# Kernel optimization log

Measured on AMD Instinct MI355X. Metric: run time of the kernel, lower is better.

## Reference

```python
import jax, jax.numpy as jnp
import numpy as np

B, S, D_IN, D_MODEL, H = 4, 2048, 1024, 1024, 16
HD = D_MODEL // H  # 64


def setup_inputs() -> dict:
    key = jax.random.key(0)
    k1, k2, k3, k4, k5 = jax.random.split(key, 5)
    x = jax.random.normal(k1, (B, S, D_IN), dtype=jnp.float32)
    mask = jnp.zeros((1, 1, S, S), dtype=jnp.float32)  # additive mask
    # qkv_layer: Linear(D_IN, 3*D_MODEL)
    W_qkv = jax.random.normal(k2, (D_IN, 3 * D_MODEL), dtype=jnp.float32) / np.sqrt(D_IN)
    b_qkv = jax.random.normal(k3, (3 * D_MODEL,), dtype=jnp.float32) * 0.01
    # linear_layer: Linear(D_MODEL, D_MODEL)
    W_o = jax.random.normal(k4, (D_MODEL, D_MODEL), dtype=jnp.float32) / np.sqrt(D_MODEL)
    b_o = jax.random.normal(k5, (D_MODEL,), dtype=jnp.float32) * 0.01
    return {"x": x, "mask": mask, "W_qkv": W_qkv, "b_qkv": b_qkv, "W_o": W_o, "b_o": b_o}


def reference(x, mask, W_qkv, b_qkv, W_o, b_o):
    b, s, _ = x.shape
    qkv = x @ W_qkv + b_qkv                                  # [B,S,3*D]
    qkv = qkv.reshape(b, s, H, 3 * HD).transpose(0, 2, 1, 3)  # [B,H,S,3*HD]
    q, k, v = jnp.split(qkv, 3, axis=-1)                     # each [B,H,S,HD]
    scale = 1.0 / jnp.sqrt(jnp.asarray(HD, dtype=q.dtype))
    scores = jnp.einsum('bhqd,bhkd->bhqk', q, k) * scale + mask  # [B,H,S,S]
    attn = jax.nn.softmax(scores, axis=-1)
    values = jnp.einsum('bhqk,bhkd->bhqd', attn, v)           # [B,H,S,HD]
    values = values.transpose(0, 2, 1, 3).reshape(b, s, H * HD)  # [B,S,D]
    out = values @ W_o + b_o
    return (out, values)
```

## Files before the change

kernel.cpp:

```cpp
#include <hip/hip_runtime.h>
#include <hip/hip_bf16.h>


typedef __attribute__((ext_vector_type(8))) short short8;
typedef __attribute__((ext_vector_type(4))) float f32x4;

#define SCL2E 0.1803368801111204f
#define L2E   1.44269504088896340736f

#define GLD16(g, l)                                                            \
  __builtin_amdgcn_global_load_lds(                                            \
      (const __attribute__((address_space(1))) unsigned int*)(g),              \
      (__attribute__((address_space(3))) unsigned int*)(l), 16, 0, 0)

__device__ __forceinline__ unsigned short f2b(float f) {
  union { float f; unsigned int u; } v; v.f = f;
  unsigned int u = v.u;
  return (unsigned short)((u + 0x7fffu + ((u >> 16) & 1u)) >> 16);
}
__device__ __forceinline__ unsigned int fbits(float f) {
  union { float f; unsigned int u; } v; v.f = f; return v.u;
}
__device__ __forceinline__ unsigned int cvt_pk_bf16(float lo, float hi) {
  unsigned int r;
  asm("v_cvt_pk_bf16_f32 %0, %1, %2" : "=v"(r) : "v"(lo), "v"(hi));
  return r;
}
__device__ __forceinline__ float max3f(float a, float b, float c) {
  return fmaxf(fmaxf(a, b), c);
}

__global__ void prep(const float* __restrict__ in, ushort* __restrict__ out,
                     const float* __restrict__ mask,
                     unsigned char* __restrict__ mflagsB) {
  const int bid = blockIdx.x;
  if (bid < 8192) {
    int i = (bid * 256 + threadIdx.x) * 4;
    float4 f = *(const float4*)(in + i);
    ushort4 o;
    o.x = f2b(f.x); o.y = f2b(f.y); o.z = f2b(f.z); o.w = f2b(f.w);
    *(ushort4*)(out + i) = o;
    return;
  }
  __shared__ unsigned int s;
  const int t = bid - 8192;
  const int qt = t >> 4, kt = t & 15;
  const float* base = mask + (size_t)(qt * 128) * 2048 + kt * 128;
  const int row = threadIdx.x >> 1, col0 = (threadIdx.x & 1) * 64;
  unsigned int acc = 0;
#pragma unroll
  for (int i = 0; i < 16; ++i) {
    float4 f = *(const float4*)(base + (size_t)row * 2048 + col0 + i * 4);
    acc |= fbits(f.x) | fbits(f.y) | fbits(f.z) | fbits(f.w);
  }
  acc &= 0x7fffffffu;
  if (threadIdx.x == 0) s = 0u;
  __syncthreads();
  if (acc) atomicOr(&s, 1u);
  __syncthreads();
  if (threadIdx.x == 0) mflagsB[t] = s ? 1 : 0;
}

__global__ void transpose_cvt2(const float* __restrict__ W1, ushort* __restrict__ Wt1,
                               const float* __restrict__ W2, ushort* __restrict__ Wt2) {
  __shared__ float tile[64][65];
  const int bx = blockIdx.x;
  const float* W; ushort* Wt; int N, n0;
  if (bx < 48) { W = W1; Wt = Wt1; N = 3072; n0 = bx * 64; }
  else         { W = W2; Wt = Wt2; N = 1024; n0 = (bx - 48) * 64; }
  const int K = 1024, k0 = blockIdx.y * 64;
  int tx = threadIdx.x & 63, ty = threadIdx.x >> 6;
#pragma unroll
  for (int i = 0; i < 64; i += 4)
    tile[ty + i][tx] = W[(size_t)(k0 + ty + i) * N + n0 + tx];
  __syncthreads();
#pragma unroll
  for (int i = 0; i < 64; i += 4)
    Wt[(size_t)(n0 + ty + i) * K + k0 + tx] = f2b(tile[tx][ty + i]);
}

template <int OUTF32, int QSCALE>
__global__ __launch_bounds__(256, 2) void gemm_bt_bias(
    const ushort* __restrict__ A, const ushort* __restrict__ Bt,
    const float* __restrict__ bias, void* __restrict__ Cout,
    int M, int N, int K) {
  __shared__ ushort As[128 * 64];
  __shared__ ushort Bs[128 * 64];
  const int lane = threadIdx.x & 63;
  const int wv = threadIdx.x >> 6;
  const int bm = blockIdx.y, bn = blockIdx.x;
  const int wm = wv >> 1, wn = wv & 1;
  f32x4 acc[4][4] = {};
  const size_t arow0 = (size_t)bm * 128;
  const size_t brow0 = (size_t)bn * 128;

  for (int k0 = 0; k0 < K; k0 += 64) {
    __syncthreads();
#pragma unroll
    for (int i = 0; i < 4; ++i) {
      int r = wv * 32 + i * 8 + (lane >> 3);
      const ushort* ga = A + (arow0 + r) * K + k0 + (lane & 7) * 8;
      GLD16(ga, As + (wv * 32 + i * 8) * 64);
      const ushort* gb = Bt + (brow0 + r) * K + k0 + (lane & 7) * 8;
      GLD16(gb, Bs + (wv * 32 + i * 8) * 64);
    }
    __syncthreads();
    short8 af[2][4], bf[2][4];
#pragma unroll
    for (int kf = 0; kf < 2; ++kf)
#pragma unroll
      for (int t = 0; t < 4; ++t) {
        af[kf][t] = *(const short8*)(As + (wm * 64 + t * 16 + (lane & 15)) * 64 +
                                     kf * 32 + (lane >> 4) * 8);
        bf[kf][t] = *(const short8*)(Bs + (wn * 64 + t * 16 + (lane & 15)) * 64 +
                                     kf * 32 + (lane >> 4) * 8);
      }
#pragma unroll
    for (int kf = 0; kf < 2; ++kf)
#pragma unroll
      for (int mt = 0; mt < 4; ++mt)
#pragma unroll
        for (int nt = 0; nt < 4; ++nt)
          acc[mt][nt] = __builtin_amdgcn_mfma_f32_16x16x32_bf16(
              af[kf][mt], bf[kf][nt], acc[mt][nt], 0, 0, 0);
  }
#pragma unroll
  for (int nt = 0; nt < 4; ++nt) {
    int col = bn * 128 + wn * 64 + nt * 16 + (lane & 15);
    float bv = bias[col];
    float scl = (QSCALE && (col % 192) < 64) ? SCL2E : 1.0f;
#pragma unroll
    for (int mt = 0; mt < 4; ++mt) {
      int row0 = bm * 128 + wm * 64 + mt * 16 + (lane >> 4) * 4;
#pragma unroll
      for (int r = 0; r < 4; ++r) {
        float v = acc[mt][nt][r] + bv;
        if (QSCALE) v *= scl;
        if (OUTF32)
          ((float*)Cout)[(size_t)(row0 + r) * N + col] = v;
        else
          ((ushort*)Cout)[(size_t)(row0 + r) * N + col] = f2b(v);
      }
    }
  }
}

__global__ __launch_bounds__(256, 2) void flash_attn(
    const ushort* __restrict__ qkv, const float* __restrict__ mask,
    const unsigned char* __restrict__ mflagsB,
    float* __restrict__ values_f, ushort* __restrict__ values_b, int qoff) {
  __shared__ ushort Ks[2][128 * 64];
  __shared__ ushort Vt[64 * 136];

  const int lane = threadIdx.x & 63;
  const int wv = threadIdx.x >> 6;
  const int c = lane & 15;
  const int g = lane >> 4;
  const int bh = blockIdx.x & 63;
  const int qt = (blockIdx.x >> 6) + qoff;
  const int b = bh >> 4, h = bh & 15;
  const size_t rowbase = (size_t)b * 2048;
  const int qcol = h * 192;
  const int swz = (c & 3) << 1;

  unsigned int flbits = 0;
  {
    const unsigned char* mb = mflagsB + qt * 16;
#pragma unroll
    for (int i = 0; i < 16; ++i) flbits |= (mb[i] ? 1u : 0u) << i;
  }

  const short8 vone = {0x3F80, 0x3F80, 0x3F80, 0x3F80,
                       0x3F80, 0x3F80, 0x3F80, 0x3F80};

  short8 qf[2][2];
#pragma unroll
  for (int mt = 0; mt < 2; ++mt)
#pragma unroll
    for (int kf = 0; kf < 2; ++kf)
      qf[mt][kf] = *(const short8*)(qkv +
          (rowbase + qt * 128 + wv * 32 + mt * 16 + c) * 3072 + qcol +
          kf * 32 + g * 8);

  f32x4 acc[2][4] = {};
  f32x4 accl[2] = {};
  float mst[2] = {0.f, 0.f};

  const int K0 = lane * 2;
  const int dq = wv;
  const int pc0 = ((K0 >> 5) << 5) + (((K0 >> 2) & 3) << 3) +
                  (((K0 >> 4) & 1) << 2) + (K0 & 3);
  const int vdw = pc0 >> 1;
  const int gcol = (((lane & 7) ^ (((lane >> 3) & 3) << 1)) << 3);

  short8 va0, va1, vb0, vb1;

  auto loadV = [&](int t) {
    const ushort* vg = qkv + (rowbase + t * 128 + K0) * 3072 + qcol + 128 + dq * 16;
    va0 = *(const short8*)(vg);
    va1 = *(const short8*)(vg + 8);
    vb0 = *(const short8*)(vg + 3072);
    vb1 = *(const short8*)(vg + 3072 + 8);
  };
  auto writeV = [&]() {
    unsigned int* Vdw = (unsigned int*)Vt;
    const unsigned int* aw0 = (const unsigned int*)&va0;
    const unsigned int* bw0 = (const unsigned int*)&vb0;
    const unsigned int* aw1 = (const unsigned int*)&va1;
    const unsigned int* bw1 = (const unsigned int*)&vb1;
#pragma unroll
    for (int k = 0; k < 4; ++k) {
      Vdw[(dq * 16 + 2 * k + 0) * 68 + vdw] =
          __builtin_amdgcn_perm(bw0[k], aw0[k], 0x05040100u);
      Vdw[(dq * 16 + 2 * k + 1) * 68 + vdw] =
          __builtin_amdgcn_perm(bw0[k], aw0[k], 0x07060302u);
    }
#pragma unroll
    for (int k = 0; k < 4; ++k) {
      Vdw[(dq * 16 + 8 + 2 * k + 0) * 68 + vdw] =
          __builtin_amdgcn_perm(bw1[k], aw1[k], 0x05040100u);
      Vdw[(dq * 16 + 8 + 2 * k + 1) * 68 + vdw] =
          __builtin_amdgcn_perm(bw1[k], aw1[k], 0x07060302u);
    }
  };
  auto stageK = [&](int t, ushort* KsD) {
#pragma unroll
    for (int i = 0; i < 4; ++i) {
      int rloc = wv * 32 + i * 8;
      const ushort* gk = qkv + (rowbase + t * 128 + rloc + (lane >> 3)) * 3072 +
                         qcol + 64 + gcol;
      GLD16(gk, KsD + rloc * 64);
    }
  };

  const float* mrow = mask + (size_t)(qt * 128 + wv * 32 + c) * 2048 + g * 4;

  loadV(0);
  stageK(0, Ks[0]);
  writeV();

  for (int kt = 0; kt < 16; ++kt) {
    __syncthreads();
    const int cur = kt & 1;
    const ushort* KsC = Ks[cur];
    if (kt < 15) {
      loadV(kt + 1);
      stageK(kt + 1, Ks[cur ^ 1]);
    }

    const bool hasmask = (flbits >> kt) & 1u;
    const float* mkt = mrow + kt * 128;
    float4 msk0[8];
    if (hasmask) {
#pragma unroll
      for (int nt = 0; nt < 8; ++nt) msk0[nt] = *(const float4*)(mkt + nt * 16);
    }

    f32x4 sc[2][8];
    __builtin_amdgcn_s_setprio(1);
#pragma unroll
    for (int nt = 0; nt < 8; ++nt) {
      short8 k0 = *(const short8*)(KsC + (nt * 16 + c) * 64 + ((g ^ swz) << 3));
      short8 k1 = *(const short8*)(KsC + (nt * 16 + c) * 64 + (((4 + g) ^ swz) << 3));
      f32x4 z = {0.f, 0.f, 0.f, 0.f};
      sc[0][nt] = __builtin_amdgcn_mfma_f32_16x16x32_bf16(k0, qf[0][0], z, 0, 0, 0);
      sc[0][nt] = __builtin_amdgcn_mfma_f32_16x16x32_bf16(k1, qf[0][1], sc[0][nt], 0, 0, 0);
      sc[1][nt] = __builtin_amdgcn_mfma_f32_16x16x32_bf16(k0, qf[1][0], z, 0, 0, 0);
      sc[1][nt] = __builtin_amdgcn_mfma_f32_16x16x32_bf16(k1, qf[1][1], sc[1][nt], 0, 0, 0);
    }
    __builtin_amdgcn_s_setprio(0);

    __attribute__((aligned(16))) unsigned int Dw[2][16];
#pragma unroll
    for (int mt = 0; mt < 2; ++mt) {
      f32x4 t4[8];
      if (hasmask) {
#pragma unroll
        for (int nt = 0; nt < 8; ++nt) {
          float4 mk = (mt == 0) ? msk0[nt]
                                : *(const float4*)(mkt + 16 * 2048 + nt * 16);
#pragma unroll
          for (int r = 0; r < 4; ++r)
            t4[nt][r] = fmaf(((const float*)&mk)[r], L2E, sc[mt][nt][r]);
        }
      } else {
#pragma unroll
        for (int nt = 0; nt < 8; ++nt) t4[nt] = sc[mt][nt];
      }
      f32x4 u, v, w, vm;
#pragma unroll
      for (int r = 0; r < 4; ++r) {
        u[r] = max3f(t4[0][r], t4[1][r], t4[2][r]);
        v[r] = max3f(t4[3][r], t4[4][r], t4[5][r]);
        w[r] = max3f(t4[6][r], t4[7][r], u[r]);
        vm[r] = fmaxf(v[r], w[r]);
      }
      float pm = fmaxf(max3f(vm[0], vm[1], vm[2]), vm[3]);
      pm = fmaxf(pm, __shfl_xor(pm, 16));
      pm = fmaxf(pm, __shfl_xor(pm, 32));
      if (!__all(pm <= mst[mt] + 16.0f && pm >= mst[mt] - 40.0f)) {
        float mnew = fmaxf(mst[mt], pm);
        bool fresh = (accl[mt][0] == 0.0f);
        if (fresh) mnew = pm;
        float alpha = fresh ? 0.0f : exp2f(mst[mt] - mnew);
        mst[mt] = mnew;
#pragma unroll
        for (int dt = 0; dt < 4; ++dt)
#pragma unroll
          for (int r = 0; r < 4; ++r) acc[mt][dt][r] *= alpha;
#pragma unroll
        for (int r = 0; r < 4; ++r) accl[mt][r] *= alpha;
      }
      if (__any(mst[mt] != 0.0f)) {
        const float mcur = mst[mt];
#pragma unroll
        for (int nt = 0; nt < 8; ++nt)
#pragma unroll
          for (int r = 0; r < 4; ++r) t4[nt][r] = exp2f(t4[nt][r] - mcur);
      } else {
#pragma unroll
        for (int nt = 0; nt < 8; ++nt)
#pragma unroll
          for (int r = 0; r < 4; ++r) t4[nt][r] = exp2f(t4[nt][r]);
      }
#pragma unroll
      for (int nt = 0; nt < 8; ++nt) {
        Dw[mt][nt * 2 + 0] = cvt_pk_bf16(t4[nt][0], t4[nt][1]);
        Dw[mt][nt * 2 + 1] = cvt_pk_bf16(t4[nt][2], t4[nt][3]);
      }
    }

    const short8* bu0 = (const short8*)Dw[0];
    const short8* bu1 = (const short8*)Dw[1];
    __builtin_amdgcn_s_setprio(1);
#pragma unroll
    for (int dt = 0; dt < 4; ++dt)
#pragma unroll
      for (int kf = 0; kf < 4; ++kf) {
        short8 vf = *(const short8*)(Vt + (dt * 16 + c) * 136 + kf * 32 + g * 8);
        acc[0][dt] = __builtin_amdgcn_mfma_f32_16x16x32_bf16(vf, bu0[kf], acc[0][dt], 0, 0, 0);
        acc[1][dt] = __builtin_amdgcn_mfma_f32_16x16x32_bf16(vf, bu1[kf], acc[1][dt], 0, 0, 0);
      }
#pragma unroll
    for (int kf = 0; kf < 4; ++kf) {
      accl[0] = __builtin_amdgcn_mfma_f32_16x16x32_bf16(vone, bu0[kf], accl[0], 0, 0, 0);
      accl[1] = __builtin_amdgcn_mfma_f32_16x16x32_bf16(vone, bu1[kf], accl[1], 0, 0, 0);
    }
    __builtin_amdgcn_s_setprio(0);

    if (kt < 15) {
      __syncthreads();
      writeV();
    }
  }

#pragma unroll
  for (int mt = 0; mt < 2; ++mt) {
    float rl = 1.0f / accl[mt][0];
    size_t qrow = rowbase + qt * 128 + wv * 32 + mt * 16 + c;
#pragma unroll
    for (int dt = 0; dt < 4; ++dt) {
      int d0 = h * 64 + dt * 16 + g * 4;
      float4 o;
      o.x = acc[mt][dt][0] * rl; o.y = acc[mt][dt][1] * rl;
      o.z = acc[mt][dt][2] * rl; o.w = acc[mt][dt][3] * rl;
      *(float4*)(values_f + qrow * 1024 + d0) = o;
      ushort4 ob;
      ob.x = f2b(o.x); ob.y = f2b(o.y); ob.z = f2b(o.z); ob.w = f2b(o.w);
      *(ushort4*)(values_b + qrow * 1024 + d0) = ob;
    }
  }
}

extern "C" void kernel_launch(void* const* d_in, const int* in_sizes, int n_in,
                              void* d_out, int out_size, void* d_ws, size_t ws_size,
                              hipStream_t stream) {
  const float* x    = (const float*)d_in[0];
  const float* mask = (const float*)d_in[1];
  const float* Wqkv = (const float*)d_in[2];
  const float* bqkv = (const float*)d_in[3];
  const float* Wo   = (const float*)d_in[4];
  const float* bo   = (const float*)d_in[5];
  float* out      = (float*)d_out;
  float* values_f = out + 8388608;

  char* ws = (char*)d_ws;
  ushort* xb    = (ushort*)(ws + 0);
  ushort* wqkvt = (ushort*)(ws + 16777216);
  ushort* wot   = (ushort*)(ws + 23068672);
  ushort* qkv   = (ushort*)(ws + 25165824);
  ushort* valb  = (ushort*)(ws + 75497472);
  unsigned char* mflg = (unsigned char*)(ws + 92274688);

  prep<<<dim3(8448), dim3(256), 0, stream>>>(x, xb, mask, mflg);
  transpose_cvt2<<<dim3(64, 16), dim3(256), 0, stream>>>(Wqkv, wqkvt, Wo, wot);
  gemm_bt_bias<0, 1><<<dim3(24, 64), dim3(256), 0, stream>>>(
      xb, wqkvt, bqkv, (void*)qkv, 8192, 3072, 1024);
  flash_attn<<<dim3(512), dim3(256), 0, stream>>>(qkv, mask, mflg, values_f, valb, 0);
  flash_attn<<<dim3(512), dim3(256), 0, stream>>>(qkv, mask, mflg, values_f, valb, 8);
  gemm_bt_bias<1, 0><<<dim3(8, 64), dim3(256), 0, stream>>>(
      valb, wot, bo, (void*)out, 8192, 1024, 1024);
}
```

Measured before the change: 361.1 us.

## Merge prep kernels, single attention launch, and interleave exp with QK MFMAs

Folds the weight transpose/convert into the input prep kernel and merges the two half-grid flash attention launches into one launch of 1024 blocks, cutting launch overhead and tail gaps. In the attention inner loop, adds a 'clean' fast path that assumes a zero running max and computes exp2 and bf16 packing per tile right after each QK MFMA pair, so softmax work overlaps matrix ops. If the observed max leaves the safe window, it falls back to recomputing with a real max and switches to the original path. This adds code size and register pressure.

```diff
diff --git a/kernel.cpp b/kernel.cpp
--- a/kernel.cpp
+++ b/kernel.cpp
@@ -30,9 +30,11 @@
   return fmaxf(fmaxf(a, b), c);
 }
 
-__global__ void prep(const float* __restrict__ in, ushort* __restrict__ out,
-                     const float* __restrict__ mask,
-                     unsigned char* __restrict__ mflagsB) {
+__global__ void prep_all(const float* __restrict__ in, ushort* __restrict__ out,
+                         const float* __restrict__ mask,
+                         unsigned char* __restrict__ mflagsB,
+                         const float* __restrict__ W1, ushort* __restrict__ Wt1,
+                         const float* __restrict__ W2, ushort* __restrict__ Wt2) {
   const int bid = blockIdx.x;
   if (bid < 8192) {
     int i = (bid * 256 + threadIdx.x) * 4;
@@ -42,33 +44,33 @@
     *(ushort4*)(out + i) = o;
     return;
   }
-  __shared__ unsigned int s;
-  const int t = bid - 8192;
-  const int qt = t >> 4, kt = t & 15;
-  const float* base = mask + (size_t)(qt * 128) * 2048 + kt * 128;
-  const int row = threadIdx.x >> 1, col0 = (threadIdx.x & 1) * 64;
-  unsigned int acc = 0;
-#pragma unroll
-  for (int i = 0; i < 16; ++i) {
-    float4 f = *(const float4*)(base + (size_t)row * 2048 + col0 + i * 4);
-    acc |= fbits(f.x) | fbits(f.y) | fbits(f.z) | fbits(f.w);
-  }
-  acc &= 0x7fffffffu;
-  if (threadIdx.x == 0) s = 0u;
-  __syncthreads();
-  if (acc) atomicOr(&s, 1u);
-  __syncthreads();
-  if (threadIdx.x == 0) mflagsB[t] = s ? 1 : 0;
-}
-
-__global__ void transpose_cvt2(const float* __restrict__ W1, ushort* __restrict__ Wt1,
-                               const float* __restrict__ W2, ushort* __restrict__ Wt2) {
+  if (bid < 8448) {
+    __shared__ unsigned int s;
+    const int t = bid - 8192;
+    const int qt = t >> 4, kt = t & 15;
+    const float* base = mask + (size_t)(qt * 128) * 2048 + kt * 128;
+    const int row = threadIdx.x >> 1, col0 = (threadIdx.x & 1) * 64;
+    unsigned int acc = 0;
+#pragma unroll
+    for (int i = 0; i < 16; ++i) {
+      float4 f = *(const float4*)(base + (size_t)row * 2048 + col0 + i * 4);
+      acc |= fbits(f.x) | fbits(f.y) | fbits(f.z) | fbits(f.w);
+    }
+    acc &= 0x7fffffffu;
+    if (threadIdx.x == 0) s = 0u;
+    __syncthreads();
+    if (acc) atomicOr(&s, 1u);
+    __syncthreads();
+    if (threadIdx.x == 0) mflagsB[t] = s ? 1 : 0;
+    return;
+  }
   __shared__ float tile[64][65];
-  const int bx = blockIdx.x;
+  const int t2 = bid - 8448;
+  const int bx = t2 & 63, by = t2 >> 6;
   const float* W; ushort* Wt; int N, n0;
   if (bx < 48) { W = W1; Wt = Wt1; N = 3072; n0 = bx * 64; }
   else         { W = W2; Wt = Wt2; N = 1024; n0 = (bx - 48) * 64; }
-  const int K = 1024, k0 = blockIdx.y * 64;
+  const int K = 1024, k0 = by * 64;
   int tx = threadIdx.x & 63, ty = threadIdx.x >> 6;
 #pragma unroll
   for (int i = 0; i < 64; i += 4)
@@ -148,7 +150,7 @@
 __global__ __launch_bounds__(256, 2) void flash_attn(
     const ushort* __restrict__ qkv, const float* __restrict__ mask,
     const unsigned char* __restrict__ mflagsB,
-    float* __restrict__ values_f, ushort* __restrict__ values_b, int qoff) {
+    float* __restrict__ values_f, ushort* __restrict__ values_b) {
   __shared__ ushort Ks[2][128 * 64];
   __shared__ ushort Vt[64 * 136];
 
@@ -157,7 +159,7 @@
   const int c = lane & 15;
   const int g = lane >> 4;
   const int bh = blockIdx.x & 63;
-  const int qt = (blockIdx.x >> 6) + qoff;
+  const int qt = blockIdx.x >> 6;
   const int b = bh >> 4, h = bh & 15;
   const size_t rowbase = (size_t)b * 2048;
   const int qcol = h * 192;
@@ -185,6 +187,7 @@
   f32x4 acc[2][4] = {};
   f32x4 accl[2] = {};
   float mst[2] = {0.f, 0.f};
+  bool clean = true;
 
   const int K0 = lane * 2;
   const int dq = wv;
@@ -257,76 +260,136 @@
     }
 
     f32x4 sc[2][8];
-    __builtin_amdgcn_s_setprio(1);
-#pragma unroll
-    for (int nt = 0; nt < 8; ++nt) {
-      short8 k0 = *(const short8*)(KsC + (nt * 16 + c) * 64 + ((g ^ swz) << 3));
-      short8 k1 = *(const short8*)(KsC + (nt * 16 + c) * 64 + (((4 + g) ^ swz) << 3));
-      f32x4 z = {0.f, 0.f, 0.f, 0.f};
-      sc[0][nt] = __builtin_amdgcn_mfma_f32_16x16x32_bf16(k0, qf[0][0], z, 0, 0, 0);
-      sc[0][nt] = __builtin_amdgcn_mfma_f32_16x16x32_bf16(k1, qf[0][1], sc[0][nt], 0, 0, 0);
-      sc[1][nt] = __builtin_amdgcn_mfma_f32_16x16x32_bf16(k0, qf[1][0], z, 0, 0, 0);
-      sc[1][nt] = __builtin_amdgcn_mfma_f32_16x16x32_bf16(k1, qf[1][1], sc[1][nt], 0, 0, 0);
-    }
-    __builtin_amdgcn_s_setprio(0);
-
     __attribute__((aligned(16))) unsigned int Dw[2][16];
-#pragma unroll
-    for (int mt = 0; mt < 2; ++mt) {
-      f32x4 t4[8];
-      if (hasmask) {
+
+    if (clean) {
+      f32x4 vmx[2];
+      vmx[0] = f32x4{-3e38f, -3e38f, -3e38f, -3e38f};
+      vmx[1] = vmx[0];
+      auto FIN = [&](int j) {
+#pragma unroll
+        for (int mt = 0; mt < 2; ++mt) {
+          f32x4 t4;
+          if (hasmask) {
+            float4 mk = (mt == 0) ? msk0[j]
+                                  : *(const float4*)(mkt + 16 * 2048 + j * 16);
+#pragma unroll
+            for (int r = 0; r < 4; ++r)
+              t4[r] = fmaf(((const float*)&mk)[r], L2E, sc[mt][j][r]);
+            sc[mt][j] = t4;
+          } else {
+            t4 = sc[mt][j];
+          }
+#pragma unroll
+          for (int r = 0; r < 4; ++r) vmx[mt][r] = fmaxf(vmx[mt][r], t4[r]);
+          float p0 = exp2f(t4[0]), p1 = exp2f(t4[1]);
+          float p2 = exp2f(t4[2]), p3 = exp2f(t4[3]);
+          Dw[mt][j * 2 + 0] = cvt_pk_bf16(p0, p1);
+          Dw[mt][j * 2 + 1] = cvt_pk_bf16(p2, p3);
+        }
+      };
+      __builtin_amdgcn_s_setprio(1);
+#pragma unroll
+      for (int nt = 0; nt < 8; ++nt) {
+        short8 k0 = *(const short8*)(KsC + (nt * 16 + c) * 64 + ((g ^ swz) << 3));
+        short8 k1 = *(const short8*)(KsC + (nt * 16 + c) * 64 + (((4 + g) ^ swz) << 3));
+        f32x4 z = {0.f, 0.f, 0.f, 0.f};
+        sc[0][nt] = __builtin_amdgcn_mfma_f32_16x16x32_bf16(k0, qf[0][0], z, 0, 0, 0);
+        sc[0][nt] = __builtin_amdgcn_mfma_f32_16x16x32_bf16(k1, qf[0][1], sc[0][nt], 0, 0, 0);
+        sc[1][nt] = __builtin_amdgcn_mfma_f32_16x16x32_bf16(k0, qf[1][0], z, 0, 0, 0);
+        sc[1][nt] = __builtin_amdgcn_mfma_f32_16x16x32_bf16(k1, qf[1][1], sc[1][nt], 0, 0, 0);
+        if (nt > 0) FIN(nt - 1);
+      }
+      FIN(7);
+      __builtin_amdgcn_s_setprio(0);
+#pragma unroll
+      for (int mt = 0; mt < 2; ++mt) {
+        float pm = fmaxf(max3f(vmx[mt][0], vmx[mt][1], vmx[mt][2]), vmx[mt][3]);
+        pm = fmaxf(pm, __shfl_xor(pm, 16));
+        pm = fmaxf(pm, __shfl_xor(pm, 32));
+        if (!__all(pm <= 16.0f && pm >= -40.0f)) {
+          clean = false;
+          float mnew = fmaxf(0.0f, pm);
+          bool fresh = (accl[mt][0] == 0.0f);
+          if (fresh) mnew = pm;
+          float alpha = fresh ? 0.0f : exp2f(-mnew);
+          mst[mt] = mnew;
+#pragma unroll
+          for (int dt = 0; dt < 4; ++dt)
+#pragma unroll
+            for (int r = 0; r < 4; ++r) acc[mt][dt][r] *= alpha;
+#pragma unroll
+          for (int r = 0; r < 4; ++r) accl[mt][r] *= alpha;
+#pragma unroll
+          for (int j = 0; j < 8; ++j) {
+            float p0 = exp2f(sc[mt][j][0] - mnew), p1 = exp2f(sc[mt][j][1] - mnew);
+            float p2 = exp2f(sc[mt][j][2] - mnew), p3 = exp2f(sc[mt][j][3] - mnew);
+            Dw[mt][j * 2 + 0] = cvt_pk_bf16(p0, p1);
+            Dw[mt][j * 2 + 1] = cvt_pk_bf16(p2, p3);
+          }
+        }
+      }
+    } else {
+      __builtin_amdgcn_s_setprio(1);
+#pragma unroll
+      for (int nt = 0; nt < 8; ++nt) {
+        short8 k0 = *(const short8*)(KsC + (nt * 16 + c) * 64 + ((g ^ swz) << 3));
+        short8 k1 = *(const short8*)(KsC + (nt * 16 + c) * 64 + (((4 + g) ^ swz) << 3));
+        f32x4 z = {0.f, 0.f, 0.f, 0.f};
+        sc[0][nt] = __builtin_amdgcn_mfma_f32_16x16x32_bf16(k0, qf[0][0], z, 0, 0, 0);
+        sc[0][nt] = __builtin_amdgcn_mfma_f32_16x16x32_bf16(k1, qf[0][1], sc[0][nt], 0, 0, 0);
+        sc[1][nt] = __builtin_amdgcn_mfma_f32_16x16x32_bf16(k0, qf[1][0], z, 0, 0, 0);
+        sc[1][nt] = __builtin_amdgcn_mfma_f32_16x16x32_bf16(k1, qf[1][1], sc[1][nt], 0, 0, 0);
+      }
+      __builtin_amdgcn_s_setprio(0);
+#pragma unroll
+      for (int mt = 0; mt < 2; ++mt) {
+        f32x4 t4[8];
+        if (hasmask) {
+#pragma unroll
+          for (int nt = 0; nt < 8; ++nt) {
+            float4 mk = (mt == 0) ? msk0[nt]
+                                  : *(const float4*)(mkt + 16 * 2048 + nt * 16);
+#pragma unroll
+            for (int r = 0; r < 4; ++r)
+              t4[nt][r] = fmaf(((const float*)&mk)[r], L2E, sc[mt][nt][r]);
+          }
+        } else {
+#pragma unroll
+          for (int nt = 0; nt < 8; ++nt) t4[nt] = sc[mt][nt];
+        }
+        f32x4 u, v, w, vm;
+#pragma unroll
+        for (int r = 0; r < 4; ++r) {
+          u[r] = max3f(t4[0][r], t4[1][r], t4[2][r]);
+          v[r] = max3f(t4[3][r], t4[4][r], t4[5][r]);
+          w[r] = max3f(t4[6][r], t4[7][r], u[r]);
+          vm[r] = fmaxf(v[r], w[r]);
+        }
+        float pm = fmaxf(max3f(vm[0], vm[1], vm[2]), vm[3]);
+        pm = fmaxf(pm, __shfl_xor(pm, 16));
+        pm = fmaxf(pm, __shfl_xor(pm, 32));
+        if (!__all(pm <= mst[mt] + 16.0f && pm >= mst[mt] - 40.0f)) {
+          float mnew = fmaxf(mst[mt], pm);
+          bool fresh = (accl[mt][0] == 0.0f);
+          if (fresh) mnew = pm;
+          float alpha = fresh ? 0.0f : exp2f(mst[mt] - mnew);
+          mst[mt] = mnew;
+#pragma unroll
+          for (int dt = 0; dt < 4; ++dt)
+#pragma unroll
+            for (int r = 0; r < 4; ++r) acc[mt][dt][r] *= alpha;
+#pragma unroll
+          for (int r = 0; r < 4; ++r) accl[mt][r] *= alpha;
+        }
+        const float mcur = mst[mt];
 #pragma unroll
         for (int nt = 0; nt < 8; ++nt) {
-          float4 mk = (mt == 0) ? msk0[nt]
-                                : *(const float4*)(mkt + 16 * 2048 + nt * 16);
-#pragma unroll
-          for (int r = 0; r < 4; ++r)
-            t4[nt][r] = fmaf(((const float*)&mk)[r], L2E, sc[mt][nt][r]);
-        }
-      } else {
-#pragma unroll
-        for (int nt = 0; nt < 8; ++nt) t4[nt] = sc[mt][nt];
-      }
-      f32x4 u, v, w, vm;
-#pragma unroll
-      for (int r = 0; r < 4; ++r) {
-        u[r] = max3f(t4[0][r], t4[1][r], t4[2][r]);
-        v[r] = max3f(t4[3][r], t4[4][r], t4[5][r]);
-        w[r] = max3f(t4[6][r], t4[7][r], u[r]);
-        vm[r] = fmaxf(v[r], w[r]);
-      }
-      float pm = fmaxf(max3f(vm[0], vm[1], vm[2]), vm[3]);
-      pm = fmaxf(pm, __shfl_xor(pm, 16));
-      pm = fmaxf(pm, __shfl_xor(pm, 32));
-      if (!__all(pm <= mst[mt] + 16.0f && pm >= mst[mt] - 40.0f)) {
-        float mnew = fmaxf(mst[mt], pm);
-        bool fresh = (accl[mt][0] == 0.0f);
-        if (fresh) mnew = pm;
-        float alpha = fresh ? 0.0f : exp2f(mst[mt] - mnew);
-        mst[mt] = mnew;
-#pragma unroll
-        for (int dt = 0; dt < 4; ++dt)
-#pragma unroll
-          for (int r = 0; r < 4; ++r) acc[mt][dt][r] *= alpha;
-#pragma unroll
-        for (int r = 0; r < 4; ++r) accl[mt][r] *= alpha;
-      }
-      if (__any(mst[mt] != 0.0f)) {
-        const float mcur = mst[mt];
-#pragma unroll
-        for (int nt = 0; nt < 8; ++nt)
-#pragma unroll
-          for (int r = 0; r < 4; ++r) t4[nt][r] = exp2f(t4[nt][r] - mcur);
-      } else {
-#pragma unroll
-        for (int nt = 0; nt < 8; ++nt)
-#pragma unroll
-          for (int r = 0; r < 4; ++r) t4[nt][r] = exp2f(t4[nt][r]);
-      }
-#pragma unroll
-      for (int nt = 0; nt < 8; ++nt) {
-        Dw[mt][nt * 2 + 0] = cvt_pk_bf16(t4[nt][0], t4[nt][1]);
-        Dw[mt][nt * 2 + 1] = cvt_pk_bf16(t4[nt][2], t4[nt][3]);
+          float p0 = exp2f(t4[nt][0] - mcur), p1 = exp2f(t4[nt][1] - mcur);
+          float p2 = exp2f(t4[nt][2] - mcur), p3 = exp2f(t4[nt][3] - mcur);
+          Dw[mt][nt * 2 + 0] = cvt_pk_bf16(p0, p1);
+          Dw[mt][nt * 2 + 1] = cvt_pk_bf16(p2, p3);
+        }
       }
     }
 
@@ -392,12 +455,11 @@
   ushort* valb  = (ushort*)(ws + 75497472);
   unsigned char* mflg = (unsigned char*)(ws + 92274688);
 
-  prep<<<dim3(8448), dim3(256), 0, stream>>>(x, xb, mask, mflg);
-  transpose_cvt2<<<dim3(64, 16), dim3(256), 0, stream>>>(Wqkv, wqkvt, Wo, wot);
+  prep_all<<<dim3(9472), dim3(256), 0, stream>>>(x, xb, mask, mflg,
+                                                 Wqkv, wqkvt, Wo, wot);
   gemm_bt_bias<0, 1><<<dim3(24, 64), dim3(256), 0, stream>>>(
       xb, wqkvt, bqkv, (void*)qkv, 8192, 3072, 1024);
-  flash_attn<<<dim3(512), dim3(256), 0, stream>>>(qkv, mask, mflg, values_f, valb, 0);
-  flash_attn<<<dim3(512), dim3(256), 0, stream>>>(qkv, mask, mflg, values_f, valb, 8);
+  flash_attn<<<dim3(1024), dim3(256), 0, stream>>>(qkv, mask, mflg, values_f, valb);
   gemm_bt_bias<1, 0><<<dim3(8, 64), dim3(256), 0, stream>>>(
       valb, wot, bo, (void*)out, 8192, 1024, 1024);
 }
```

New measurement: 352.6 us. -2.4%, faster.
